# Performance work log

Measured on AMD Instinct MI355X. Metric: run time of the kernel, lower is better.

The kernel has to match this reference:

```python
import jax, jax.numpy as jnp
import numpy as np

EMBED = 128   # embed_dim
HEADS = 8
POINTS = 4
H_SP, W_SP = 51, 102   # hardcoded spatial_shapes in __init__
BEV = 100              # bev_res
HRES = 50              # height_res


def _make_ref_points():
    """Exact numpy replica of the spherical grid built in __init__."""
    eps = 1e-6
    x = np.linspace(-71 / 2, 71 / 2, BEV)
    y = np.linspace(-71 / 2, 71 / 2, BEV)
    z = np.linspace(-50 / 2, 50 / 2, HRES)
    gx, gy, gz = np.meshgrid(x, y, z, indexing='ij')
    phi = np.sign(gy + eps) * np.arccos(gx / (np.sqrt(gx ** 2 + gy ** 2) + eps))
    theta = np.arccos(gz / (np.sqrt(gx ** 2 + gy ** 2 + gz ** 2) + eps))
    phi = 2 * np.pi - phi
    phi[phi > 2 * np.pi] -= 2 * np.pi
    col = phi / (2 * np.pi)   # grd_col_cross
    row = theta / np.pi       # grd_row_cross
    ref = np.stack([col, row], axis=-1)              # (BEV, BEV, HRES, 2)
    ref = ref.transpose(2, 0, 1, 3).reshape(HRES, BEV * BEV, 2)
    return jnp.asarray(ref, dtype=jnp.float32)


def setup_inputs() -> dict:
    key = jax.random.key(0)
    ks = jax.random.split(key, 12)
    d = EMBED
    s = 0.02
    return {
        'query': jax.random.normal(ks[0], (1, BEV * BEV, d), jnp.float32),
        'value': jax.random.normal(ks[1], (1, H_SP * W_SP, d), jnp.float32),
        'ref_points': _make_ref_points(),
        'W_off': jax.random.normal(ks[2], (d, HEADS * POINTS * 2), jnp.float32) * s,
        'b_off': jax.random.normal(ks[3], (HEADS * POINTS * 2,), jnp.float32) * s,
        'W_attn': jax.random.normal(ks[4], (d, HEADS * POINTS), jnp.float32) * s,
        'b_attn': jax.random.normal(ks[5], (HEADS * POINTS,), jnp.float32) * s,
        'W_val': jax.random.normal(ks[6], (d, d), jnp.float32) * s,
        'b_val': jax.random.normal(ks[7], (d,), jnp.float32) * s,
        'W_out': jax.random.normal(ks[8], (d, d), jnp.float32) * s,
        'b_out': jax.random.normal(ks[9], (d,), jnp.float32) * s,
        'W_proj': jax.random.normal(ks[10], (d, 1), jnp.float32) * s,
        'b_proj': jax.random.normal(ks[11], (1,), jnp.float32) * s,
    }


def _bilinear_sample(vflat, loc):
    """grid_sample(bilinear, zero padding, align_corners=False).
    vflat: (B, H*W, hd) value maps; loc: (B, N, 2) normalized [0,1] (x,y)."""
    px = loc[..., 0] * W_SP - 0.5
    py = loc[..., 1] * H_SP - 0.5
    x0 = jnp.floor(px)
    y0 = jnp.floor(py)
    dx = (px - x0)[..., None]
    dy = (py - y0)[..., None]
    x0i = x0.astype(jnp.int32)
    y0i = y0.astype(jnp.int32)

    def gather(xi, yi):
        valid = (xi >= 0) & (xi < W_SP) & (yi >= 0) & (yi < H_SP)
        idx = jnp.clip(yi, 0, H_SP - 1) * W_SP + jnp.clip(xi, 0, W_SP - 1)
        v = jnp.take_along_axis(vflat, idx[..., None], axis=1)  # (B, N, hd)
        return v * valid[..., None].astype(vflat.dtype)

    v00 = gather(x0i, y0i)
    v01 = gather(x0i + 1, y0i)
    v10 = gather(x0i, y0i + 1)
    v11 = gather(x0i + 1, y0i + 1)
    return (v00 * (1 - dx) * (1 - dy) + v01 * dx * (1 - dy)
            + v10 * (1 - dx) * dy + v11 * dx * dy)


def reference(query, value, ref_points, W_off, b_off, W_attn, b_attn,
              W_val, b_val, W_out, b_out, W_proj, b_proj):
    bs, nq, d = query.shape
    hd = d // HEADS
    L = ref_points.shape[0]

    # query-dependent MSDA projections (identical across height levels)
    offsets = (query @ W_off + b_off).reshape(bs, nq, HEADS, POINTS, 2)
    aw = jax.nn.softmax((query @ W_attn + b_attn).reshape(bs, nq, HEADS, POINTS), axis=-1)
    awt = aw.transpose(0, 2, 1, 3)                              # (bs, heads, nq, points)
    v = (value @ W_val + b_val).reshape(bs, -1, HEADS, hd)
    vflat = v.transpose(0, 2, 1, 3).reshape(bs * HEADS, H_SP * W_SP, hd)
    norm = jnp.asarray([W_SP, H_SP], dtype=query.dtype)         # offset_normalizer [W, H]

    def per_level(ref):  # ref: (nq, 2) -> MSDA output with its internal residual
        loc = ref[None, :, None, None, :] + offsets / norm      # (bs, nq, heads, pts, 2)
        loc = loc.transpose(0, 2, 1, 3, 4).reshape(bs * HEADS, nq * POINTS, 2)
        samp = _bilinear_sample(vflat, loc).reshape(bs, HEADS, nq, POINTS, hd)
        out = jnp.einsum('bhnp,bhnpd->bnhd', awt, samp).reshape(bs, nq, d)
        return out @ W_out + b_out + query                      # mmcv MSDA adds identity

    grd = jax.vmap(per_level)(ref_points)                       # (L, bs, nq, d)
    grd_3d = grd.transpose(1, 2, 0, 3).reshape(bs, BEV, BEV, L, d)
    weights = jax.nn.softmax(grd_3d @ W_proj + b_proj, axis=3)  # (bs, BEV, BEV, L, 1)
    max_height_index = jnp.argmax(weights, axis=3)              # (bs, BEV, BEV, 1)
    grd_bev = (weights * grd_3d).sum(axis=3)                    # (bs, BEV, BEV, d)
    return grd_bev.reshape(bs, nq, d) + query, max_height_index
```

## Files before the change

kernel.cpp:

```cpp
#include <hip/hip_runtime.h>
#include <math.h>

#define EMBED   128
#define NHEADS  8
#define NPOINTS 4
#define HD      16
#define HSP     51
#define WSP     102
#define NPIX    (HSP * WSP)
#define NQ      10000
#define NLVL    50

#define NPB_A ((NPIX + 1) / 2)
#define NPB_B (NQ / 2)

__global__ __launch_bounds__(256) void k_prep(
    const float* __restrict__ value,
    const float* __restrict__ Wv,
    const float* __restrict__ bv,
    const float* __restrict__ query,
    const float* __restrict__ Woff,
    const float* __restrict__ boff,
    const float* __restrict__ Wattn,
    const float* __restrict__ battn,
    const float* __restrict__ Wout,
    const float* __restrict__ Wproj,
    float* __restrict__ vout,
    float* __restrict__ off_out,
    float* __restrict__ aw_out,
    float* __restrict__ u_out) {
    const int b = blockIdx.x;
    const int t = threadIdx.x;
    const int unit = t >> 7;
    const int tt = t & 127;

    if (b < NPB_A) {
        __shared__ float vrow[2][EMBED];
        const int pix = b * 2 + unit;
        vrow[unit][tt] = value[(size_t)pix * EMBED + tt];
        __syncthreads();
        float acc = bv[tt];
        const float* vr = vrow[unit];
#pragma unroll 8
        for (int k = 0; k < EMBED; ++k)
            acc = fmaf(vr[k], Wv[(size_t)k * EMBED + tt], acc);
        const int h = tt >> 4, c = tt & 15;
        vout[((size_t)h * NPIX + pix) * HD + c] = acc;
    } else if (b < NPB_A + NPB_B) {
        const int q = (b - NPB_A) * 2 + unit;
        __shared__ float qrow[2][EMBED];
        __shared__ float attn[2][32];
        qrow[unit][tt] = query[(size_t)q * EMBED + tt];
        __syncthreads();
        const float* qr = qrow[unit];
        if (tt < 64) {
            float acc = boff[tt];
#pragma unroll 8
            for (int k = 0; k < EMBED; ++k)
                acc = fmaf(qr[k], Woff[(size_t)k * 64 + tt], acc);
            off_out[(size_t)q * 64 + tt] = acc;
        } else if (tt < 96) {
            const int j = tt - 64;
            float acc = battn[j];
#pragma unroll 8
            for (int k = 0; k < EMBED; ++k)
                acc = fmaf(qr[k], Wattn[(size_t)k * 32 + j], acc);
            attn[unit][j] = acc;
        }
        __syncthreads();
        if (tt < NHEADS) {
            const float a0 = attn[unit][tt * 4 + 0], a1 = attn[unit][tt * 4 + 1];
            const float a2 = attn[unit][tt * 4 + 2], a3 = attn[unit][tt * 4 + 3];
            const float mx = fmaxf(fmaxf(a0, a1), fmaxf(a2, a3));
            const float e0 = __expf(a0 - mx), e1 = __expf(a1 - mx);
            const float e2 = __expf(a2 - mx), e3 = __expf(a3 - mx);
            const float inv = 1.f / (e0 + e1 + e2 + e3);
            aw_out[(size_t)q * 32 + tt * 4 + 0] = e0 * inv;
            aw_out[(size_t)q * 32 + tt * 4 + 1] = e1 * inv;
            aw_out[(size_t)q * 32 + tt * 4 + 2] = e2 * inv;
            aw_out[(size_t)q * 32 + tt * 4 + 3] = e3 * inv;
        }
    } else {
        if (unit == 0) {
            float acc = 0.f;
#pragma unroll 8
            for (int d = 0; d < EMBED; ++d)
                acc = fmaf(Wout[(size_t)tt * EMBED + d], Wproj[d], acc);
            u_out[tt] = acc;
        }
    }
}

__global__ __launch_bounds__(256, 6) void k_main(
    const float* __restrict__ query,
    const float* __restrict__ refp,
    const float* __restrict__ voff,
    const float* __restrict__ vaw,
    const float* __restrict__ vflat,
    const float* __restrict__ uvec,
    const float* __restrict__ Wout,
    const float* __restrict__ bout,
    float* __restrict__ out0,
    float* __restrict__ out1) {
    const int t = threadIdx.x;
    const int qslot = t >> 7;
    const int w2 = (t >> 6) & 1;
    const int half = (t >> 5) & 1;
    const int sub = t & 31;
    const int h  = sub >> 2;
    const int c4 = sub & 3;
    const int q = blockIdx.x * 2 + qslot;

    __shared__ float  s_rpy[2][NLVL];
    __shared__ float4 s_acc[2][32];
    __shared__ float  s_z[2], s_m[2];
    __shared__ int    s_b[2];

    if (t < 2 * NLVL) {
        const int ql = t / NLVL, l = t - ql * NLVL;
        const int qq = blockIdx.x * 2 + ql;
        s_rpy[ql][l] = refp[((size_t)l * NQ + qq) * 2 + 1];
    }

    const float4* offp = (const float4*)(voff + (size_t)q * 64 + h * 8);
    const float4 o01 = offp[0];
    const float4 o23 = offp[1];
    const float4 awv4 = *(const float4*)(vaw + (size_t)q * 32 + h * 4);
    const float4 u4 = *(const float4*)(uvec + h * 16 + c4 * 4);
    const float rpx = refp[(size_t)q * 2];
    const float4* vbase = (const float4*)vflat + (size_t)h * NPIX * 4 + c4;

    const float offx[4] = {o01.x, o01.z, o23.x, o23.z};
    const float offy[4] = {o01.y, o01.w, o23.y, o23.w};
    const float awv[4]  = {awv4.x, awv4.y, awv4.z, awv4.w};

    float wx0[NPOINTS], wx1[NPOINTS], oyc[NPOINTS];
    int xo0[NPOINTS], xo1[NPOINTS];
#pragma unroll
    for (int p = 0; p < NPOINTS; ++p) {
        const float px = fmaf(rpx, (float)WSP, offx[p]) - 0.5f;
        const float fx = floorf(px);
        const float dx = px - fx;
        const int x0 = (int)fx, x1 = x0 + 1;
        const float a = awv[p];
        wx0[p] = ((unsigned)x0 < (unsigned)WSP) ? a * (1.f - dx) : 0.f;
        wx1[p] = ((unsigned)x1 < (unsigned)WSP) ? a * dx : 0.f;
        xo0[p] = min(max(x0, 0), WSP - 1) * 4;
        xo1[p] = min(max(x1, 0), WSP - 1) * 4;
        oyc[p] = offy[p] - 0.5f;
    }

    __syncthreads();

    float4 acc = {0.f, 0.f, 0.f, 0.f};
    float Z = 0.f, m = -1e30f;
    int best = 0;

#pragma unroll 1
    for (int i = 0; i < 13; ++i) {
        if (4 * i + (w2 << 1) >= NLVL) break;
        const int l = 4 * i + (w2 << 1) + half;
        const float rpy = s_rpy[qslot][l];
        float4 s = {0.f, 0.f, 0.f, 0.f};
#pragma unroll
        for (int p = 0; p < NPOINTS; ++p) {
            const float py = fmaf(rpy, (float)HSP, oyc[p]);
            const float fy = floorf(py);
            const float dy = py - fy;
            const int y0 = (int)fy, y1 = y0 + 1;
            const float t0 = ((unsigned)y0 < (unsigned)HSP) ? (1.f - dy) : 0.f;
            const float t1 = ((unsigned)y1 < (unsigned)HSP) ? dy : 0.f;
            const int rb0 = min(max(y0, 0), HSP - 1) * (WSP * 4);
            const int rb1 = min(max(y1, 0), HSP - 1) * (WSP * 4);
            const float w00 = wx0[p] * t0;
            const float w01 = wx1[p] * t0;
            const float w10 = wx0[p] * t1;
            const float w11 = wx1[p] * t1;
            const float4 v00 = vbase[rb0 + xo0[p]];
            const float4 v01 = vbase[rb0 + xo1[p]];
            const float4 v10 = vbase[rb1 + xo0[p]];
            const float4 v11 = vbase[rb1 + xo1[p]];
            s.x = fmaf(w00, v00.x, s.x); s.y = fmaf(w00, v00.y, s.y);
            s.z = fmaf(w00, v00.z, s.z); s.w = fmaf(w00, v00.w, s.w);
            s.x = fmaf(w01, v01.x, s.x); s.y = fmaf(w01, v01.y, s.y);
            s.z = fmaf(w01, v01.z, s.z); s.w = fmaf(w01, v01.w, s.w);
            s.x = fmaf(w10, v10.x, s.x); s.y = fmaf(w10, v10.y, s.y);
            s.z = fmaf(w10, v10.z, s.z); s.w = fmaf(w10, v10.w, s.w);
            s.x = fmaf(w11, v11.x, s.x); s.y = fmaf(w11, v11.y, s.y);
            s.z = fmaf(w11, v11.z, s.z); s.w = fmaf(w11, v11.w, s.w);
        }
        float part = s.x * u4.x;
        part = fmaf(s.y, u4.y, part);
        part = fmaf(s.z, u4.z, part);
        part = fmaf(s.w, u4.w, part);
#pragma unroll
        for (int d = 1; d < 32; d <<= 1)
            part += __shfl_xor(part, d, 64);
        const float e = __expf(part);
        Z += e;
        acc.x = fmaf(e, s.x, acc.x);
        acc.y = fmaf(e, s.y, acc.y);
        acc.z = fmaf(e, s.z, acc.z);
        acc.w = fmaf(e, s.w, acc.w);
        best = (part > m) ? l : best;
        m = fmaxf(part, m);
    }

    {
        const float mo = __shfl_xor(m, 32, 64);
        const int   bo = __shfl_xor(best, 32, 64);
        const float Zo = __shfl_xor(Z, 32, 64);
        const float ax = __shfl_xor(acc.x, 32, 64);
        const float ay = __shfl_xor(acc.y, 32, 64);
        const float az = __shfl_xor(acc.z, 32, 64);
        const float aw_ = __shfl_xor(acc.w, 32, 64);
        const bool takeOther = (mo > m) || (mo == m && bo < best);
        best = takeOther ? bo : best;
        m = fmaxf(m, mo);
        Z += Zo;
        acc.x += ax; acc.y += ay; acc.z += az; acc.w += aw_;
    }

    if (w2 == 1) {
        if (half == 0) s_acc[qslot][sub] = acc;
        if ((t & 63) == 0) { s_z[qslot] = Z; s_m[qslot] = m; s_b[qslot] = best; }
    }
    __syncthreads();

    if (w2 == 0) {
        const float4 ao = s_acc[qslot][sub];
        const float Zo = s_z[qslot];
        const float mo = s_m[qslot];
        const int   bo = s_b[qslot];
        const bool takeOther = (mo > m) || (mo == m && bo < best);
        best = takeOther ? bo : best;
        Z += Zo;
        acc.x += ao.x; acc.y += ao.y; acc.z += ao.z; acc.w += ao.w;

        const float inv = 1.f / Z;
        if (half == 0) {
            float4 sv;
            sv.x = acc.x * inv; sv.y = acc.y * inv;
            sv.z = acc.z * inv; sv.w = acc.w * inv;
            s_acc[qslot][sub] = sv;
            if (sub == 0) out1[q] = (float)best;
        }

        const int dpb = sub * 4;
        float4 r = {0.f, 0.f, 0.f, 0.f};
        if (half == 0) {
            const float4 b4 = *(const float4*)(bout + dpb);
            const float4 q4 = *(const float4*)(query + (size_t)q * EMBED + dpb);
            r.x = fmaf(2.f, q4.x, b4.x);
            r.y = fmaf(2.f, q4.y, b4.y);
            r.z = fmaf(2.f, q4.z, b4.z);
            r.w = fmaf(2.f, q4.w, b4.w);
        }
        const float4* srow = s_acc[qslot];
        const int cg0 = half * 16;
#pragma unroll 4
        for (int cg = cg0; cg < cg0 + 16; ++cg) {
            const float4 s4 = srow[cg];
            const float4 w0 = *(const float4*)(Wout + (size_t)(cg * 4 + 0) * EMBED + dpb);
            const float4 w1 = *(const float4*)(Wout + (size_t)(cg * 4 + 1) * EMBED + dpb);
            const float4 w2v = *(const float4*)(Wout + (size_t)(cg * 4 + 2) * EMBED + dpb);
            const float4 w3 = *(const float4*)(Wout + (size_t)(cg * 4 + 3) * EMBED + dpb);
            r.x = fmaf(s4.x, w0.x, r.x); r.y = fmaf(s4.x, w0.y, r.y);
            r.z = fmaf(s4.x, w0.z, r.z); r.w = fmaf(s4.x, w0.w, r.w);
            r.x = fmaf(s4.y, w1.x, r.x); r.y = fmaf(s4.y, w1.y, r.y);
            r.z = fmaf(s4.y, w1.z, r.z); r.w = fmaf(s4.y, w1.w, r.w);
            r.x = fmaf(s4.z, w2v.x, r.x); r.y = fmaf(s4.z, w2v.y, r.y);
            r.z = fmaf(s4.z, w2v.z, r.z); r.w = fmaf(s4.z, w2v.w, r.w);
            r.x = fmaf(s4.w, w3.x, r.x); r.y = fmaf(s4.w, w3.y, r.y);
            r.z = fmaf(s4.w, w3.z, r.z); r.w = fmaf(s4.w, w3.w, r.w);
        }
        {
            const float rx = __shfl_xor(r.x, 32, 64);
            const float ry = __shfl_xor(r.y, 32, 64);
            const float rz = __shfl_xor(r.z, 32, 64);
            const float rw = __shfl_xor(r.w, 32, 64);
            r.x += rx; r.y += ry; r.z += rz; r.w += rw;
        }
        if (half == 0)
            *(float4*)(out0 + (size_t)q * EMBED + dpb) = r;
    }
}

extern "C" void kernel_launch(void* const* d_in, const int* in_sizes, int n_in,
                              void* d_out, int out_size, void* d_ws, size_t ws_size,
                              hipStream_t stream) {
    const float* query = (const float*)d_in[0];
    const float* value = (const float*)d_in[1];
    const float* refp  = (const float*)d_in[2];
    const float* Woff  = (const float*)d_in[3];
    const float* boff  = (const float*)d_in[4];
    const float* Wattn = (const float*)d_in[5];
    const float* battn = (const float*)d_in[6];
    const float* Wval  = (const float*)d_in[7];
    const float* bval  = (const float*)d_in[8];
    const float* Wout  = (const float*)d_in[9];
    const float* bout  = (const float*)d_in[10];
    const float* Wproj = (const float*)d_in[11];

    float* ws = (float*)d_ws;
    float* ws_v   = ws;
    float* ws_off = ws_v + (size_t)NHEADS * NPIX * HD;
    float* ws_aw  = ws_off + (size_t)NQ * 64;
    float* ws_u   = ws_aw + (size_t)NQ * 32;

    float* out0 = (float*)d_out;
    float* out1 = out0 + (size_t)NQ * EMBED;

    hipLaunchKernelGGL(k_prep, dim3(NPB_A + NPB_B + 1), dim3(256), 0, stream,
                       value, Wval, bval, query, Woff, boff, Wattn, battn,
                       Wout, Wproj, ws_v, ws_off, ws_aw, ws_u);
    hipLaunchKernelGGL(k_main, dim3(NQ / 2), dim3(256), 0, stream,
                       query, refp, ws_off, ws_aw, ws_v, ws_u, Wout, bout,
                       out0, out1);
}
```

Baseline: 253.1 us.

## Store value maps in fp16 and recheck near-tie argmax with fp32 fix pass

```diff
diff --git a/kernel.cpp b/kernel.cpp
--- a/kernel.cpp
+++ b/kernel.cpp
@@ -1,4 +1,5 @@
 #include <hip/hip_runtime.h>
+#include <hip/hip_fp16.h>
 #include <math.h>
 
 #define EMBED   128
@@ -10,6 +11,7 @@
 #define NPIX    (HSP * WSP)
 #define NQ      10000
 #define NLVL    50
+#define TAU     2.0e-4f
 
 #define NPB_A ((NPIX + 1) / 2)
 #define NPB_B (NQ / 2)
@@ -25,7 +27,8 @@
     const float* __restrict__ battn,
     const float* __restrict__ Wout,
     const float* __restrict__ Wproj,
-    float* __restrict__ vout,
+    __half* __restrict__ vh,
+    float* __restrict__ gfield,
     float* __restrict__ off_out,
     float* __restrict__ aw_out,
     float* __restrict__ u_out) {
@@ -36,6 +39,7 @@
 
     if (b < NPB_A) {
         __shared__ float vrow[2][EMBED];
+        __shared__ float gprod[2][EMBED];
         const int pix = b * 2 + unit;
         vrow[unit][tt] = value[(size_t)pix * EMBED + tt];
         __syncthreads();
@@ -44,8 +48,22 @@
 #pragma unroll 8
         for (int k = 0; k < EMBED; ++k)
             acc = fmaf(vr[k], Wv[(size_t)k * EMBED + tt], acc);
+        float ut = 0.f;
+#pragma unroll 8
+        for (int d = 0; d < EMBED; ++d)
+            ut = fmaf(Wout[(size_t)tt * EMBED + d], Wproj[d], ut);
         const int h = tt >> 4, c = tt & 15;
-        vout[((size_t)h * NPIX + pix) * HD + c] = acc;
+        vh[((size_t)h * NPIX + pix) * HD + c] = __float2half(acc);
+        gprod[unit][tt] = acc * ut;
+        __syncthreads();
+        if (t < 16) {
+            const int u2 = t >> 3, h2 = t & 7;
+            float s = 0.f;
+#pragma unroll
+            for (int c2 = 0; c2 < HD; ++c2)
+                s += gprod[u2][h2 * HD + c2];
+            gfield[(size_t)h2 * NPIX + b * 2 + u2] = s;
+        }
     } else if (b < NPB_A + NPB_B) {
         const int q = (b - NPB_A) * 2 + unit;
         __shared__ float qrow[2][EMBED];
@@ -91,110 +109,103 @@
     }
 }
 
-__global__ __launch_bounds__(256, 6) void k_main(
+__global__ __launch_bounds__(256, 8) void k_main(
     const float* __restrict__ query,
     const float* __restrict__ refp,
     const float* __restrict__ voff,
     const float* __restrict__ vaw,
-    const float* __restrict__ vflat,
+    const __half* __restrict__ vh,
     const float* __restrict__ uvec,
     const float* __restrict__ Wout,
     const float* __restrict__ bout,
     float* __restrict__ out0,
-    float* __restrict__ out1) {
+    float* __restrict__ out1,
+    int* __restrict__ cnt,
+    int* __restrict__ list) {
     const int t = threadIdx.x;
-    const int qslot = t >> 7;
-    const int w2 = (t >> 6) & 1;
-    const int half = (t >> 5) & 1;
-    const int sub = t & 31;
-    const int h  = sub >> 2;
-    const int c4 = sub & 3;
-    const int q = blockIdx.x * 2 + qslot;
-
-    __shared__ float  s_rpy[2][NLVL];
-    __shared__ float4 s_acc[2][32];
-    __shared__ float  s_z[2], s_m[2];
-    __shared__ int    s_b[2];
-
-    if (t < 2 * NLVL) {
-        const int ql = t / NLVL, l = t - ql * NLVL;
-        const int qq = blockIdx.x * 2 + ql;
-        s_rpy[ql][l] = refp[((size_t)l * NQ + qq) * 2 + 1];
-    }
-
-    const float4* offp = (const float4*)(voff + (size_t)q * 64 + h * 8);
-    const float4 o01 = offp[0];
-    const float4 o23 = offp[1];
-    const float4 awv4 = *(const float4*)(vaw + (size_t)q * 32 + h * 4);
-    const float4 u4 = *(const float4*)(uvec + h * 16 + c4 * 4);
+    const int w = t >> 6;
+    const int lane = t & 63;
+    const int h  = lane >> 3;
+    const int xc = (lane >> 2) & 1;
+    const int c4 = lane & 3;
+    const int q = blockIdx.x;
+
+    __shared__ float  s_rpy[NLVL];
+    __shared__ float4 s_pub[3][32];
+    __shared__ float  s_ms[3], s_m2s[3], s_zs[3];
+    __shared__ int    s_bs[3];
+    __shared__ float4 s_sv[32];
+
+    if (t < NLVL) s_rpy[t] = refp[((size_t)t * NQ + q) * 2 + 1];
+
+    const float4 o01 = *(const float4*)(voff + (size_t)q * 64 + h * 8);
+    const float4 o23 = *(const float4*)(voff + (size_t)q * 64 + h * 8 + 4);
+    const float4 aw4 = *(const float4*)(vaw + (size_t)q * 32 + h * 4);
+    const float4 u4  = *(const float4*)(uvec + h * 16 + c4 * 4);
     const float rpx = refp[(size_t)q * 2];
-    const float4* vbase = (const float4*)vflat + (size_t)h * NPIX * 4 + c4;
 
     const float offx[4] = {o01.x, o01.z, o23.x, o23.z};
     const float offy[4] = {o01.y, o01.w, o23.y, o23.w};
-    const float awv[4]  = {awv4.x, awv4.y, awv4.z, awv4.w};
-
-    float wx0[NPOINTS], wx1[NPOINTS], oyc[NPOINTS];
-    int xo0[NPOINTS], xo1[NPOINTS];
+    const float aww[4]  = {aw4.x, aw4.y, aw4.z, aw4.w};
+
+    float wlx[NPOINTS], oyc[NPOINTS];
+    int xpix[NPOINTS];
 #pragma unroll
     for (int p = 0; p < NPOINTS; ++p) {
         const float px = fmaf(rpx, (float)WSP, offx[p]) - 0.5f;
         const float fx = floorf(px);
         const float dx = px - fx;
-        const int x0 = (int)fx, x1 = x0 + 1;
-        const float a = awv[p];
-        wx0[p] = ((unsigned)x0 < (unsigned)WSP) ? a * (1.f - dx) : 0.f;
-        wx1[p] = ((unsigned)x1 < (unsigned)WSP) ? a * dx : 0.f;
-        xo0[p] = min(max(x0, 0), WSP - 1) * 4;
-        xo1[p] = min(max(x1, 0), WSP - 1) * 4;
+        const int xi = (int)fx + xc;
+        const float wx = xc ? dx : (1.f - dx);
+        wlx[p] = ((unsigned)xi < (unsigned)WSP) ? aww[p] * wx : 0.f;
+        xpix[p] = min(max(xi, 0), WSP - 1);
         oyc[p] = offy[p] - 0.5f;
     }
+    const __half* vbase = vh + (size_t)h * NPIX * HD + c4 * 4;
 
     __syncthreads();
 
     float4 acc = {0.f, 0.f, 0.f, 0.f};
-    float Z = 0.f, m = -1e30f;
+    float Z = 0.f, m = -1e30f, m2 = -1e30f;
     int best = 0;
 
 #pragma unroll 1
     for (int i = 0; i < 13; ++i) {
-        if (4 * i + (w2 << 1) >= NLVL) break;
-        const int l = 4 * i + (w2 << 1) + half;
-        const float rpy = s_rpy[qslot][l];
+        const int l = 4 * i + w;
+        if (l >= NLVL) break;
+        const float rpy = s_rpy[l];
         float4 s = {0.f, 0.f, 0.f, 0.f};
 #pragma unroll
         for (int p = 0; p < NPOINTS; ++p) {
             const float py = fmaf(rpy, (float)HSP, oyc[p]);
             const float fy = floorf(py);
             const float dy = py - fy;
-            const int y0 = (int)fy, y1 = y0 + 1;
+            const int y0 = (int)fy;
             const float t0 = ((unsigned)y0 < (unsigned)HSP) ? (1.f - dy) : 0.f;
-            const float t1 = ((unsigned)y1 < (unsigned)HSP) ? dy : 0.f;
-            const int rb0 = min(max(y0, 0), HSP - 1) * (WSP * 4);
-            const int rb1 = min(max(y1, 0), HSP - 1) * (WSP * 4);
-            const float w00 = wx0[p] * t0;
-            const float w01 = wx1[p] * t0;
-            const float w10 = wx0[p] * t1;
-            const float w11 = wx1[p] * t1;
-            const float4 v00 = vbase[rb0 + xo0[p]];
-            const float4 v01 = vbase[rb0 + xo1[p]];
-            const float4 v10 = vbase[rb1 + xo0[p]];
-            const float4 v11 = vbase[rb1 + xo1[p]];
-            s.x = fmaf(w00, v00.x, s.x); s.y = fmaf(w00, v00.y, s.y);
-            s.z = fmaf(w00, v00.z, s.z); s.w = fmaf(w00, v00.w, s.w);
-            s.x = fmaf(w01, v01.x, s.x); s.y = fmaf(w01, v01.y, s.y);
-            s.z = fmaf(w01, v01.z, s.z); s.w = fmaf(w01, v01.w, s.w);
-            s.x = fmaf(w10, v10.x, s.x); s.y = fmaf(w10, v10.y, s.y);
-            s.z = fmaf(w10, v10.z, s.z); s.w = fmaf(w10, v10.w, s.w);
-            s.x = fmaf(w11, v11.x, s.x); s.y = fmaf(w11, v11.y, s.y);
-            s.z = fmaf(w11, v11.z, s.z); s.w = fmaf(w11, v11.w, s.w);
+            const float t1 = ((unsigned)(y0 + 1) < (unsigned)HSP) ? dy : 0.f;
+            const int rb0 = min(max(y0, 0), HSP - 1) * WSP;
+            const int rb1 = min(max(y0 + 1, 0), HSP - 1) * WSP;
+            const float w0 = wlx[p] * t0;
+            const float w1 = wlx[p] * t1;
+            const __half2* p0 = (const __half2*)(vbase + (size_t)(rb0 + xpix[p]) * HD);
+            const __half2* p1 = (const __half2*)(vbase + (size_t)(rb1 + xpix[p]) * HD);
+            const __half2 h00 = p0[0], h01 = p0[1];
+            const __half2 h10 = p1[0], h11 = p1[1];
+            const float2 a0 = __half22float2(h00);
+            const float2 a1 = __half22float2(h01);
+            const float2 b0 = __half22float2(h10);
+            const float2 b1 = __half22float2(h11);
+            s.x = fmaf(w0, a0.x, s.x); s.y = fmaf(w0, a0.y, s.y);
+            s.z = fmaf(w0, a1.x, s.z); s.w = fmaf(w0, a1.y, s.w);
+            s.x = fmaf(w1, b0.x, s.x); s.y = fmaf(w1, b0.y, s.y);
+            s.z = fmaf(w1, b1.x, s.z); s.w = fmaf(w1, b1.y, s.w);
         }
         float part = s.x * u4.x;
         part = fmaf(s.y, u4.y, part);
         part = fmaf(s.z, u4.z, part);
         part = fmaf(s.w, u4.w, part);
 #pragma unroll
-        for (int d = 1; d < 32; d <<= 1)
+        for (int d = 1; d < 64; d <<= 1)
             part += __shfl_xor(part, d, 64);
         const float e = __expf(part);
         Z += e;
@@ -202,50 +213,54 @@
         acc.y = fmaf(e, s.y, acc.y);
         acc.z = fmaf(e, s.z, acc.z);
         acc.w = fmaf(e, s.w, acc.w);
-        best = (part > m) ? l : best;
-        m = fmaxf(part, m);
-    }
-
-    {
-        const float mo = __shfl_xor(m, 32, 64);
-        const int   bo = __shfl_xor(best, 32, 64);
-        const float Zo = __shfl_xor(Z, 32, 64);
-        const float ax = __shfl_xor(acc.x, 32, 64);
-        const float ay = __shfl_xor(acc.y, 32, 64);
-        const float az = __shfl_xor(acc.z, 32, 64);
-        const float aw_ = __shfl_xor(acc.w, 32, 64);
-        const bool takeOther = (mo > m) || (mo == m && bo < best);
-        best = takeOther ? bo : best;
-        m = fmaxf(m, mo);
-        Z += Zo;
-        acc.x += ax; acc.y += ay; acc.z += az; acc.w += aw_;
-    }
-
-    if (w2 == 1) {
-        if (half == 0) s_acc[qslot][sub] = acc;
-        if ((t & 63) == 0) { s_z[qslot] = Z; s_m[qslot] = m; s_b[qslot] = best; }
+        if (part > m) { m2 = m; m = part; best = l; }
+        else          { m2 = fmaxf(m2, part); }
+    }
+
+    acc.x += __shfl_xor(acc.x, 4, 64);
+    acc.y += __shfl_xor(acc.y, 4, 64);
+    acc.z += __shfl_xor(acc.z, 4, 64);
+    acc.w += __shfl_xor(acc.w, 4, 64);
+
+    if (w > 0) {
+        if (xc == 0) s_pub[w - 1][h * 4 + c4] = acc;
+        if (lane == 0) {
+            s_ms[w - 1] = m; s_m2s[w - 1] = m2;
+            s_zs[w - 1] = Z; s_bs[w - 1] = best;
+        }
     }
     __syncthreads();
 
-    if (w2 == 0) {
-        const float4 ao = s_acc[qslot][sub];
-        const float Zo = s_z[qslot];
-        const float mo = s_m[qslot];
-        const int   bo = s_b[qslot];
-        const bool takeOther = (mo > m) || (mo == m && bo < best);
-        best = takeOther ? bo : best;
-        Z += Zo;
-        acc.x += ao.x; acc.y += ao.y; acc.z += ao.z; acc.w += ao.w;
-
+    if (w == 0) {
+        const int hc = h * 4 + c4;
+#pragma unroll
+        for (int j = 0; j < 3; ++j) {
+            const float4 ao = s_pub[j][hc];
+            const float mo = s_ms[j], m2o = s_m2s[j], Zo = s_zs[j];
+            const int bo = s_bs[j];
+            const bool takeOther = (mo > m) || (mo == m && bo < best);
+            m2 = fmaxf(fmaxf(m2, m2o), fminf(m, mo));
+            best = takeOther ? bo : best;
+            m = fmaxf(m, mo);
+            Z += Zo;
+            acc.x += ao.x; acc.y += ao.y; acc.z += ao.z; acc.w += ao.w;
+        }
         const float inv = 1.f / Z;
-        if (half == 0) {
+        if (xc == 0) {
             float4 sv;
             sv.x = acc.x * inv; sv.y = acc.y * inv;
             sv.z = acc.z * inv; sv.w = acc.w * inv;
-            s_acc[qslot][sub] = sv;
-            if (sub == 0) out1[q] = (float)best;
-        }
-
+            s_sv[hc] = sv;
+        }
+        if (lane == 0) {
+            out1[q] = (float)best;
+            if (m - m2 < TAU) {
+                const int ii = atomicAdd(cnt, 1);
+                list[ii] = q;
+            }
+        }
+        const int sub = lane & 31;
+        const int half = lane >> 5;
         const int dpb = sub * 4;
         float4 r = {0.f, 0.f, 0.f, 0.f};
         if (half == 0) {
@@ -256,11 +271,10 @@
             r.z = fmaf(2.f, q4.z, b4.z);
             r.w = fmaf(2.f, q4.w, b4.w);
         }
-        const float4* srow = s_acc[qslot];
         const int cg0 = half * 16;
 #pragma unroll 4
         for (int cg = cg0; cg < cg0 + 16; ++cg) {
-            const float4 s4 = srow[cg];
+            const float4 s4 = s_sv[cg];
             const float4 w0 = *(const float4*)(Wout + (size_t)(cg * 4 + 0) * EMBED + dpb);
             const float4 w1 = *(const float4*)(Wout + (size_t)(cg * 4 + 1) * EMBED + dpb);
             const float4 w2v = *(const float4*)(Wout + (size_t)(cg * 4 + 2) * EMBED + dpb);
@@ -283,6 +297,69 @@
         }
         if (half == 0)
             *(float4*)(out0 + (size_t)q * EMBED + dpb) = r;
+    }
+}
+
+__global__ __launch_bounds__(64) void k_fix(
+    const float* __restrict__ refp,
+    const float* __restrict__ voff,
+    const float* __restrict__ vaw,
+    const float* __restrict__ gfield,
+    const int* __restrict__ cnt,
+    const int* __restrict__ list,
+    float* __restrict__ out1) {
+    const int n = *cnt;
+    const int lane = threadIdx.x;
+    for (int idx = blockIdx.x; idx < n; idx += gridDim.x) {
+        const int q = list[idx];
+        float logit = -1e30f;
+        if (lane < NLVL) {
+            const float rpx = refp[(size_t)q * 2];
+            const float rpy = refp[((size_t)lane * NQ + q) * 2 + 1];
+            float accl = 0.f;
+            for (int h = 0; h < NHEADS; ++h) {
+                const float4 o01 = *(const float4*)(voff + (size_t)q * 64 + h * 8);
+                const float4 o23 = *(const float4*)(voff + (size_t)q * 64 + h * 8 + 4);
+                const float4 aw4 = *(const float4*)(vaw + (size_t)q * 32 + h * 4);
+                const float* gh = gfield + (size_t)h * NPIX;
+                const float offx[4] = {o01.x, o01.z, o23.x, o23.z};
+                const float offy[4] = {o01.y, o01.w, o23.y, o23.w};
+                const float aww[4]  = {aw4.x, aw4.y, aw4.z, aw4.w};
+#pragma unroll
+                for (int p = 0; p < NPOINTS; ++p) {
+                    const float px = fmaf(rpx, (float)WSP, offx[p]) - 0.5f;
+                    const float py = fmaf(rpy, (float)HSP, offy[p]) - 0.5f;
+                    const float fx = floorf(px), fy = floorf(py);
+                    const float dx = px - fx, dy = py - fy;
+                    const int x0 = (int)fx, y0 = (int)fy;
+                    const float wx0 = ((unsigned)x0 < (unsigned)WSP) ? (1.f - dx) : 0.f;
+                    const float wx1 = ((unsigned)(x0 + 1) < (unsigned)WSP) ? dx : 0.f;
+                    const float t0 = ((unsigned)y0 < (unsigned)HSP) ? (1.f - dy) : 0.f;
+                    const float t1 = ((unsigned)(y0 + 1) < (unsigned)HSP) ? dy : 0.f;
+                    const int xc0 = min(max(x0, 0), WSP - 1);
+                    const int xc1 = min(max(x0 + 1, 0), WSP - 1);
+                    const int rb0 = min(max(y0, 0), HSP - 1) * WSP;
+                    const int rb1 = min(max(y0 + 1, 0), HSP - 1) * WSP;
+                    const float g00 = gh[rb0 + xc0];
+                    const float g01 = gh[rb0 + xc1];
+                    const float g10 = gh[rb1 + xc0];
+                    const float g11 = gh[rb1 + xc1];
+                    const float bil = wx0 * t0 * g00 + wx1 * t0 * g01
+                                    + wx0 * t1 * g10 + wx1 * t1 * g11;
+                    accl = fmaf(aww[p], bil, accl);
+                }
+            }
+            logit = accl;
+        }
+        float v = logit;
+        int b = lane;
+#pragma unroll
+        for (int d = 1; d < 64; d <<= 1) {
+            const float vo = __shfl_xor(v, d, 64);
+            const int bo = __shfl_xor(b, d, 64);
+            if ((vo > v) || (vo == v && bo < b)) { v = vo; b = bo; }
+        }
+        if (lane == 0) out1[q] = (float)b;
     }
 }
 
@@ -303,18 +380,24 @@
     const float* Wproj = (const float*)d_in[11];
 
     float* ws = (float*)d_ws;
-    float* ws_v   = ws;
-    float* ws_off = ws_v + (size_t)NHEADS * NPIX * HD;
+    __half* ws_vh = (__half*)ws;
+    float* ws_g   = ws + ((size_t)NHEADS * NPIX * HD + 1) / 2;
+    float* ws_off = ws_g + (size_t)NHEADS * NPIX;
     float* ws_aw  = ws_off + (size_t)NQ * 64;
     float* ws_u   = ws_aw + (size_t)NQ * 32;
+    int*   ws_cnt = (int*)(ws_u + 128);
+    int*   ws_list = ws_cnt + 1;
 
     float* out0 = (float*)d_out;
     float* out1 = out0 + (size_t)NQ * EMBED;
 
+    hipMemsetAsync(ws_cnt, 0, sizeof(int), stream);
     hipLaunchKernelGGL(k_prep, dim3(NPB_A + NPB_B + 1), dim3(256), 0, stream,
                        value, Wval, bval, query, Woff, boff, Wattn, battn,
-                       Wout, Wproj, ws_v, ws_off, ws_aw, ws_u);
-    hipLaunchKernelGGL(k_main, dim3(NQ / 2), dim3(256), 0, stream,
-                       query, refp, ws_off, ws_aw, ws_v, ws_u, Wout, bout,
-                       out0, out1);
+                       Wout, Wproj, ws_vh, ws_g, ws_off, ws_aw, ws_u);
+    hipLaunchKernelGGL(k_main, dim3(NQ), dim3(256), 0, stream,
+                       query, refp, ws_off, ws_aw, ws_vh, ws_u, Wout, bout,
+                       out0, out1, ws_cnt, ws_list);
+    hipLaunchKernelGGL(k_fix, dim3(256), dim3(64), 0, stream,
+                       refp, ws_off, ws_aw, ws_g, ws_cnt, ws_list, out1);
 }
```

Result: slower. 390.5 us (+54.3%).
